# Kernel tuning notes

Measured on AMD Instinct MI355X. Metric: run time of the kernel, lower is better.

The kernel has to match this reference:

```python
import jax, jax.numpy as jnp
import numpy as np

NUM_CLASSES = 21
TOP_K = 200
CONF_THRESH = 0.01
NMS_THRESH = 0.045
VAR0, VAR1 = 0.1, 0.2  # SSD decode variances
B, N = 128, 8732  # batch, num anchors (SSD300)


def setup_inputs() -> dict:
    key = jax.random.key(0)
    k1, k2, k3 = jax.random.split(key, 3)
    loc = jax.random.normal(k1, (B, N, 4), jnp.float32)
    conf = jax.random.normal(k2, (B, N, NUM_CLASSES), jnp.float32)
    # anchors in center-size form (cx, cy, w, h), values in (0,1)
    anchors = jax.random.uniform(k3, (N, 4), jnp.float32)
    return {"loc": loc, "conf": conf, "anchors": anchors}


def decode(loc, anchors):
    # loc [N,4], anchors [N,4] (cx,cy,w,h) -> corner boxes [N,4]
    cxcy = anchors[:, :2] + loc[:, :2] * VAR0 * anchors[:, 2:]
    wh = anchors[:, 2:] * jnp.exp(loc[:, 2:] * VAR1)
    return jnp.concatenate([cxcy - 0.5 * wh, cxcy + 0.5 * wh], axis=-1)


def pairwise_iou(boxes):
    # boxes [K,4] -> IoU [K,K]
    lt = jnp.maximum(boxes[:, None, :2], boxes[None, :, :2])
    rb = jnp.minimum(boxes[:, None, 2:], boxes[None, :, 2:])
    wh = jnp.clip(rb - lt, 0.0)
    inter = wh[..., 0] * wh[..., 1]
    area = (boxes[:, 2] - boxes[:, 0]) * (boxes[:, 3] - boxes[:, 1])
    return inter / (area[:, None] + area[None, :] - inter + 1e-12)


def nms_one_class(scores, boxes):
    # scores [N], boxes [N,4] -> packed [TOP_K, 5] (score, x1,y1,x2,y2)
    masked = jnp.where(scores > CONF_THRESH, scores, 0.0)
    top_s, idx = jax.lax.top_k(masked, TOP_K)
    top_b = boxes[idx]                      # [K,4]
    iou = pairwise_iou(top_b)               # [K,K]
    ar = jnp.arange(TOP_K)
    def body(i, keep):
        sup = keep[i] & (iou[i] > NMS_THRESH) & (ar > i)
        return keep & ~sup
    keep = jax.lax.fori_loop(0, TOP_K, body, top_s > CONF_THRESH)
    # pack kept detections to the front (stable sort preserves score order)
    order = jnp.argsort(jnp.logical_not(keep))
    ent = jnp.concatenate([top_s[:, None], top_b], axis=-1)[order]
    return jnp.where(keep[order][:, None], ent, 0.0)


def reference(loc, conf, anchors):
    probs = jax.nn.softmax(conf, axis=-1)   # [B,N,C]
    def per_image(loc_i, probs_i):
        boxes = decode(loc_i, anchors)      # [N,4]
        return jax.vmap(lambda s: nms_one_class(s, boxes))(probs_i.T)  # [C,K,5]
    out = jax.vmap(per_image)(loc, probs)   # [B,C,K,5]
    return out.at[:, 0].set(0.0)            # class 0 = background, left zero
```

## Files before the change

### kernel.cpp

```cpp
#include <hip/hip_runtime.h>
#include <math.h>

#pragma clang fp contract(off)

#define NB 128
#define NA 8732
#define NC 21
#define TOPK 200
#define BCAP 512
#define CONF_T 0.01
#define NMS_T 0.045
#define NQ (NA / 4)
#define HSIZE 1024

__device__ __forceinline__ double exact_score_cf(const float* __restrict__ conf,
                                                 int b, int i, int c) {
  const float* row = conf + ((size_t)b * NA + i) * NC;
  float r[NC];
#pragma unroll
  for (int k = 0; k < NC; ++k) r[k] = row[k];
  float mx = r[0];
#pragma unroll
  for (int k = 1; k < NC; ++k) mx = fmaxf(mx, r[k]);
  double d = 0.0;
#pragma unroll
  for (int k = 0; k < NC; ++k) d += exp((double)r[k] - (double)mx);
  double s = exp((double)r[c] - (double)mx) / d;
  return (s > CONF_T) ? s : 0.0;
}

__device__ __forceinline__ double exact_score_aux(const float* __restrict__ conf,
                                                  const float* __restrict__ mxa,
                                                  const double* __restrict__ da,
                                                  int b, int i, int c) {
  size_t r = (size_t)b * NA + i;
  double v = (double)conf[r * NC + c];
  double m = (double)mxa[r];
  double s = exp(v - m) / da[r];
  return (s > CONF_T) ? s : 0.0;
}

__device__ __forceinline__ double exact_score(const float* __restrict__ conf,
                                              const float* __restrict__ mxa,
                                              const double* __restrict__ da,
                                              int use_aux, int b, int i, int c) {
  if (use_aux) return exact_score_aux(conf, mxa, da, b, i, c);
  return exact_score_cf(conf, b, i, c);
}

__device__ __forceinline__ void decode64(const float* __restrict__ loc,
                                         const float* __restrict__ anchors,
                                         int b, int ai, double* o) {
  const float* lp = loc + ((size_t)b * NA + ai) * 4;
  const float* ap = anchors + (size_t)ai * 4;
  double l0 = (double)lp[0], l1 = (double)lp[1];
  double l2 = (double)lp[2], l3 = (double)lp[3];
  double a0 = (double)ap[0], a1 = (double)ap[1];
  double a2 = (double)ap[2], a3 = (double)ap[3];
  double cx = a0 + (l0 * 0.1) * a2;
  double cy = a1 + (l1 * 0.1) * a3;
  double w = a2 * exp(l2 * 0.2);
  double h = a3 * exp(l3 * 0.2);
  o[0] = cx - 0.5 * w; o[1] = cy - 0.5 * h;
  o[2] = cx + 0.5 * w; o[3] = cy + 0.5 * h;
}

__device__ __forceinline__ bool entBefore(double sa, int ia, double sb, int ib) {
  return (sa > sb) || (sa == sb && ia < ib);
}

__device__ __forceinline__ int kbucket(unsigned key) {
  if (key == 0u) return -1;
  int x = (int)(key >> 16) - 0x3C00 + 1;
  if (x < 1) x = 1;
  if (x > HSIZE - 1) x = HSIZE - 1;
  return x;
}

__global__ __launch_bounds__(256) void k_prep(const float* __restrict__ conf,
                                              float* __restrict__ scores,
                                              float* __restrict__ mxout,
                                              double* __restrict__ dout,
                                              int do_aux) {
  __shared__ float rows[256 * NC];
  int base = blockIdx.x * 256;
  const float4* src = (const float4*)(conf + (size_t)base * NC);
  float4* dst = (float4*)rows;
  for (int t = threadIdx.x; t < (256 * NC) / 4; t += 256) dst[t] = src[t];
  __syncthreads();
  int g = base + threadIdx.x;
  const float* row = rows + threadIdx.x * NC;
  float v[NC];
#pragma unroll
  for (int k = 0; k < NC; ++k) v[k] = row[k];
  float mx = v[0];
#pragma unroll
  for (int k = 1; k < NC; ++k) mx = fmaxf(mx, v[k]);
  float e[NC], s = 0.0f;
#pragma unroll
  for (int k = 0; k < NC; ++k) {
    e[k] = expf(v[k] - mx);
    s += e[k];
  }
  float inv = 1.0f / s;
  int b = g / NA, i = g - b * NA;
#pragma unroll
  for (int cc = 1; cc < NC; ++cc) {
    float sc = e[cc] * inv;
    scores[(size_t)(b * (NC - 1) + (cc - 1)) * NA + i] = (sc > 0.0099f) ? sc : 0.0f;
  }
  if (do_aux) {
    double d = 0.0;
#pragma unroll
    for (int k = 0; k < NC; ++k) d += exp((double)v[k] - (double)mx);
    mxout[g] = mx;
    dout[g] = d;
  }
}

__global__ __launch_bounds__(256, 8) void k_fast(const float* __restrict__ loc,
                                                 const float* __restrict__ conf,
                                                 const float* __restrict__ anchors,
                                                 const float* __restrict__ scores,
                                                 const float* __restrict__ mxa,
                                                 const double* __restrict__ da,
                                                 float* __restrict__ out,
                                                 int use_aux) {
  int id = blockIdx.x;
  int xcd = id & 7, slot = id >> 3;
  int c = slot % NC;
  int b = (slot / NC) * 8 + xcd;
  int tid = threadIdx.x;
  float* outbase = out + ((size_t)(b * NC + c)) * TOPK * 5;

  if (c == 0) {
    for (int k = tid; k < TOPK * 5; k += 256) outbase[k] = 0.0f;
    return;
  }

  __shared__ unsigned hist[HSIZE];
  __shared__ unsigned chunk[256];
  __shared__ unsigned chunk2[32];
  union U2 {
    struct { double bnds[BCAP]; int bndi[BCAP]; } bb;
    double dbox[TOPK][4];
  };
  __shared__ U2 u2;
  __shared__ float4 fbox[TOPK];
  __shared__ float farea[TOPK];
  __shared__ double ssel[256];
  __shared__ int isel[256];
  __shared__ unsigned keepw[7];
  __shared__ int ctl_cnt, ctl_m, ctl_n1, ctl_kneed, ctl_lo, ctl_hi, ctl_k;
  __shared__ unsigned ctl_pref;

  const float4* sc4 =
      (const float4*)(scores + (size_t)(b * (NC - 1) + (c - 1)) * NA);

  for (int t = tid; t < HSIZE; t += 256) hist[t] = 0u;
  if (tid == 0) { ctl_cnt = 0; ctl_m = 0; }
  __syncthreads();
  for (int q = tid; q < NQ; q += 256) {
    float4 k4 = sc4[q];
    unsigned kb[4] = {__float_as_uint(k4.x), __float_as_uint(k4.y),
                      __float_as_uint(k4.z), __float_as_uint(k4.w)};
#pragma unroll
    for (int t = 0; t < 4; ++t) {
      int idx = kbucket(kb[t]);
      if (idx >= 0) atomicAdd(&hist[idx], 1u);
    }
  }
  __syncthreads();

  {
    unsigned csum = 0;
#pragma unroll
    for (int j = 0; j < 4; ++j) csum += hist[tid * 4 + j];
    chunk[tid] = csum;
  }
  __syncthreads();
  if (tid < 32) {
    unsigned s = 0;
#pragma unroll
    for (int j = 0; j < 8; ++j) s += chunk[tid * 8 + j];
    chunk2[tid] = s;
  }
  __syncthreads();
  if (tid == 0) {
    unsigned cum = 0;
    int t2 = -1;
    for (int t = 31; t >= 0; --t) {
      unsigned h = chunk2[t];
      if (cum + h >= (unsigned)TOPK) { t2 = t; break; }
      cum += h;
    }
    if (t2 < 0) {
      ctl_lo = 1; ctl_hi = 0; ctl_n1 = (int)cum; ctl_kneed = TOPK - (int)cum;
    } else {
      int tc = t2 * 8;
      for (int t = t2 * 8 + 7; t >= t2 * 8; --t) {
        unsigned h = chunk[t];
        if (cum + h >= (unsigned)TOPK) { tc = t; break; }
        cum += h;
      }
      int D = tc * 4;
      for (int j = tc * 4 + 3; j >= tc * 4; --j) {
        unsigned h = hist[j];
        if (cum + h >= (unsigned)TOPK) { D = j; break; }
        cum += h;
      }
      int hi = (D + 1 < HSIZE) ? D + 1 : D;
      int lo = (D - 1 >= 1) ? D - 1 : D;
      unsigned hup = (hi > D) ? hist[hi] : 0u;
      ctl_lo = lo; ctl_hi = hi;
      ctl_n1 = (int)(cum - hup);
      ctl_kneed = TOPK - ctl_n1;
    }
  }
  __syncthreads();
  int lo = ctl_lo, hi = ctl_hi, n1 = ctl_n1, kneed = ctl_kneed;

  {
    unsigned tCert = (unsigned)(0x3C00 + hi) << 16;
    unsigned tBnd = (unsigned)(0x3BFF + lo) << 16;
    for (int q = tid; q < NQ; q += 256) {
      float4 k4 = sc4[q];
      unsigned kb[4] = {__float_as_uint(k4.x), __float_as_uint(k4.y),
                        __float_as_uint(k4.z), __float_as_uint(k4.w)};
#pragma unroll
      for (int t = 0; t < 4; ++t) {
        unsigned key = kb[t];
        if (key >= tCert) {
          int p = atomicAdd(&ctl_cnt, 1);
          if (p < 256) isel[p] = q * 4 + t;
        } else if (key >= tBnd) {
          int p = atomicAdd(&ctl_m, 1);
          if (p < BCAP) u2.bb.bndi[p] = q * 4 + t;
        }
      }
    }
  }
  __syncthreads();
  int m = (hi > 0) ? ctl_m : 0;

  if (hi > 0 && m > BCAP) {
    if (tid == 0) { ctl_k = TOPK; ctl_pref = 0u; }
    __syncthreads();
    for (int shift = 24; shift >= 0; shift -= 8) {
      hist[tid] = 0u;
      __syncthreads();
      unsigned pref = ctl_pref;
      for (int q = tid; q < NQ; q += 256) {
        float4 k4 = sc4[q];
        unsigned kb[4] = {__float_as_uint(k4.x), __float_as_uint(k4.y),
                          __float_as_uint(k4.z), __float_as_uint(k4.w)};
#pragma unroll
        for (int t = 0; t < 4; ++t) {
          unsigned key = kb[t];
          if (key == 0u) continue;
          bool match = (shift == 24) || ((key >> (shift + 8)) == (pref >> (shift + 8)));
          if (match) atomicAdd(&hist[(key >> shift) & 255u], 1u);
        }
      }
      __syncthreads();
      if (tid == 0) {
        int k = ctl_k;
        unsigned cum = 0;
        int d = 255;
        for (; d > 0; --d) {
          unsigned h = hist[d];
          if (cum + h >= (unsigned)k) break;
          cum += h;
        }
        ctl_k = k - (int)cum;
        ctl_pref = pref | ((unsigned)d << shift);
      }
      __syncthreads();
    }
    unsigned Tf = ctl_pref;
    kneed = ctl_k;
    n1 = TOPK - kneed;
    if (tid == 0) { ctl_cnt = 0; ctl_m = 0; }
    __syncthreads();
    for (int q = tid; q < NQ; q += 256) {
      float4 k4 = sc4[q];
      unsigned kb[4] = {__float_as_uint(k4.x), __float_as_uint(k4.y),
                        __float_as_uint(k4.z), __float_as_uint(k4.w)};
#pragma unroll
      for (int t = 0; t < 4; ++t) {
        unsigned key = kb[t];
        if (key > Tf) {
          int p = atomicAdd(&ctl_cnt, 1);
          if (p < 256) isel[p] = q * 4 + t;
        } else if (key == Tf) {
          int p = atomicAdd(&ctl_m, 1);
          if (p < BCAP) u2.bb.bndi[p] = q * 4 + t;
        }
      }
    }
    __syncthreads();
    m = ctl_m;
    if (m > BCAP) m = BCAP;
  }

  if (hi > 0) {
    for (int q = tid; q < m; q += 256)
      u2.bb.bnds[q] = exact_score(conf, mxa, da, use_aux, b, u2.bb.bndi[q], c);
    __syncthreads();
    for (int q = tid; q < m; q += 256) {
      double sq = u2.bb.bnds[q];
      int iq = u2.bb.bndi[q];
      int rank = 0;
      for (int r = 0; r < m; ++r)
        if (entBefore(u2.bb.bnds[r], u2.bb.bndi[r], sq, iq)) ++rank;
      if (rank < kneed) { isel[n1 + rank] = iq; ssel[n1 + rank] = sq; }
    }
  } else {
    for (int j = n1 + tid; j < TOPK; j += 256) {
      isel[j] = j - n1;
      ssel[j] = 0.0;
    }
  }
  __syncthreads();

  if (tid < TOPK) {
    if (tid < n1) ssel[tid] = exact_score(conf, mxa, da, use_aux, b, isel[tid], c);
  } else {
    ssel[tid] = -1.0;
    isel[tid] = 0x7fffffff;
  }

  for (int kk = 2; kk <= 256; kk <<= 1) {
    for (int j = kk >> 1; j > 0; j >>= 1) {
      __syncthreads();
      int ixj = tid ^ j;
      if (ixj > tid) {
        double s1 = ssel[tid], s2 = ssel[ixj];
        int i1 = isel[tid], i2 = isel[ixj];
        bool up = ((tid & kk) == 0);
        bool sw = up ? entBefore(s2, i2, s1, i1) : entBefore(s1, i1, s2, i2);
        if (sw) {
          ssel[tid] = s2; ssel[ixj] = s1;
          isel[tid] = i2; isel[ixj] = i1;
        }
      }
    }
  }
  __syncthreads();

  double dx1 = 0, dy1 = 0, dx2 = 0, dy2 = 0;
  if (tid < TOPK) {
    double bx[4];
    decode64(loc, anchors, b, isel[tid], bx);
    dx1 = bx[0]; dy1 = bx[1]; dx2 = bx[2]; dy2 = bx[3];
    fbox[tid] = make_float4((float)dx1, (float)dy1, (float)dx2, (float)dy2);
    farea[tid] = (float)((dx2 - dx1) * (dy2 - dy1));
    u2.dbox[tid][0] = dx1; u2.dbox[tid][1] = dy1;
    u2.dbox[tid][2] = dx2; u2.dbox[tid][3] = dy2;
  }
  __syncthreads();

  if (tid < 64) {
    int l = tid;
    unsigned kr = 0u;
    float4 ob[4]; float oa[4];
#pragma unroll
    for (int q = 0; q < 4; ++q) {
      int j = l + 64 * q;
      if (j < TOPK) {
        if (ssel[j] > CONF_T) kr |= 1u << q;
        ob[q] = fbox[j];
        oa[q] = farea[j];
      } else {
        ob[q] = make_float4(0.0f, 0.0f, 0.0f, 0.0f);
        oa[q] = 0.0f;
      }
    }
    int cur = 0;
    while (cur < TOPK) {
      unsigned long long ms0 = __ballot((int)(kr & 1u));
      unsigned long long ms1 = __ballot((int)(kr & 2u));
      unsigned long long ms2 = __ballot((int)(kr & 4u));
      unsigned long long ms3 = __ballot((int)(kr & 8u));
      int q0 = cur >> 6;
      int sh = cur & 63;
      unsigned long long below = sh ? ((1ull << sh) - 1ull) : 0ull;
      unsigned long long t0 = (q0 == 0) ? (ms0 & ~below) : 0ull;
      unsigned long long t1 = (q0 < 1) ? ms1 : ((q0 == 1) ? (ms1 & ~below) : 0ull);
      unsigned long long t2 = (q0 < 2) ? ms2 : ((q0 == 2) ? (ms2 & ~below) : 0ull);
      unsigned long long t3 = (q0 < 3) ? ms3 : (ms3 & ~below);
      int i = TOPK;
      if (t0) i = __ffsll(t0) - 1;
      else if (t1) i = 64 + __ffsll(t1) - 1;
      else if (t2) i = 128 + __ffsll(t2) - 1;
      else if (t3) i = 192 + __ffsll(t3) - 1;
      if (i >= TOPK) break;
      float4 fbi = fbox[i];
      float fai = farea[i];
#pragma unroll
      for (int q = 0; q < 4; ++q) {
        int r = l + 64 * q;
        if (r > i && r < TOPK && ((kr >> q) & 1u)) {
          float lx = fmaxf(fbi.x, ob[q].x), ly = fmaxf(fbi.y, ob[q].y);
          float rx = fminf(fbi.z, ob[q].z), ry = fminf(fbi.w, ob[q].w);
          float iw = fmaxf(rx - lx, 0.0f), ih = fmaxf(ry - ly, 0.0f);
          float inter = iw * ih;
          float uni = fai + oa[q] - inter + 1e-12f;
          float diff = inter - 0.045f * uni;
          bool sup;
          if (fabsf(diff) < 3e-4f * uni) {
            double ix1 = u2.dbox[i][0], iy1 = u2.dbox[i][1];
            double ix2 = u2.dbox[i][2], iy2 = u2.dbox[i][3];
            double jx1 = u2.dbox[r][0], jy1 = u2.dbox[r][1];
            double jx2 = u2.dbox[r][2], jy2 = u2.dbox[r][3];
            double dlx = fmax(ix1, jx1), dly = fmax(iy1, jy1);
            double drx = fmin(ix2, jx2), dry = fmin(iy2, jy2);
            double diw = drx - dlx; if (diw < 0.0) diw = 0.0;
            double dih = dry - dly; if (dih < 0.0) dih = 0.0;
            double dint = diw * dih;
            double dai = (ix2 - ix1) * (iy2 - iy1);
            double daj = (jx2 - jx1) * (jy2 - jy1);
            sup = dint > NMS_T * (dai + daj - dint + 1e-12);
          } else {
            sup = diff > 0.0f;
          }
          if (sup) kr &= ~(1u << q);
        }
      }
      cur = i + 1;
    }
#pragma unroll
    for (int q = 0; q < 4; ++q) {
      unsigned long long bal = __ballot((int)((kr >> q) & 1u));
      if (l == 0) {
        keepw[2 * q] = (unsigned)bal;
        if (2 * q + 1 < 7) keepw[2 * q + 1] = (unsigned)(bal >> 32);
      }
    }
  }
  __syncthreads();

  int nk = 0;
#pragma unroll
  for (int w = 0; w < 7; ++w) nk += __popc(keepw[w]);
  if (tid < TOPK) {
    int j = tid;
    bool kept = (keepw[j >> 5] >> (j & 31)) & 1u;
    if (kept) {
      int pos = 0;
      for (int w = 0; w < (j >> 5); ++w) pos += __popc(keepw[w]);
      pos += __popc(keepw[j >> 5] & ((1u << (j & 31)) - 1u));
      float* o = outbase + (size_t)pos * 5;
      o[0] = (float)ssel[j];
      o[1] = (float)dx1;
      o[2] = (float)dy1;
      o[3] = (float)dx2;
      o[4] = (float)dy2;
    }
    if (j >= nk) {
      float* o = outbase + (size_t)j * 5;
      o[0] = 0.0f; o[1] = 0.0f; o[2] = 0.0f; o[3] = 0.0f; o[4] = 0.0f;
    }
  }
}

__global__ __launch_bounds__(256) void k_main_nf(const float* __restrict__ loc,
                                                 const float* __restrict__ conf,
                                                 const float* __restrict__ anchors,
                                                 float* __restrict__ out) {
  int bc = blockIdx.x;
  int b = bc / NC;
  int c = bc % NC;
  int tid = threadIdx.x;
  float* outbase = out + (size_t)bc * TOPK * 5;
  if (c == 0) {
    for (int k = tid; k < TOPK * 5; k += 256) outbase[k] = 0.0f;
    return;
  }
  union U {
    float sf[NA];
    struct { double box[TOPK][4]; double area[TOPK]; } p2;
  };
  __shared__ U u;
  __shared__ double ssel[256];
  __shared__ int isel[256];
  __shared__ unsigned hist[256];
  __shared__ double bnds[256];
  __shared__ int bndi[256];
  __shared__ int keepL[256];
  __shared__ unsigned long long wmask[4];
  __shared__ int ctl_k, ctl_cnt, ctl_m;
  __shared__ unsigned ctl_pref;

  for (int i = tid; i < NA; i += 256)
    u.sf[i] = (float)exact_score_cf(conf, b, i, c);
  if (tid == 0) { ctl_k = TOPK; ctl_pref = 0u; }
  __syncthreads();
  for (int shift = 24; shift >= 0; shift -= 8) {
    hist[tid] = 0u;
    __syncthreads();
    unsigned pref = ctl_pref;
    for (int i = tid; i < NA; i += 256) {
      unsigned key = __float_as_uint(u.sf[i]);
      bool match = (shift == 24) || ((key >> (shift + 8)) == (pref >> (shift + 8)));
      if (match) atomicAdd(&hist[(key >> shift) & 255u], 1u);
    }
    __syncthreads();
    if (tid == 0) {
      int k = ctl_k;
      unsigned cum = 0;
      int d = 255;
      for (; d > 0; --d) {
        unsigned h = hist[d];
        if (cum + h >= (unsigned)k) break;
        cum += h;
      }
      ctl_k = k - (int)cum;
      ctl_pref = pref | ((unsigned)d << shift);
    }
    __syncthreads();
  }
  unsigned Tf = ctl_pref;
  int kneed = ctl_k;
  int n1 = TOPK - kneed;
  if (tid == 0) { ctl_cnt = 0; ctl_m = 0; }
  __syncthreads();
  for (int i = tid; i < NA; i += 256) {
    unsigned key = __float_as_uint(u.sf[i]);
    if (key > Tf) {
      int p = atomicAdd(&ctl_cnt, 1);
      if (p < 256) isel[p] = i;
    } else if (key == Tf && Tf != 0u) {
      int q = atomicAdd(&ctl_m, 1);
      if (q < 256) bndi[q] = i;
    }
  }
  __syncthreads();
  int zf;
  if (Tf == 0u) {
    zf = n1;
    for (int j = n1 + tid; j < TOPK; j += 256) isel[j] = j - n1;
  } else {
    zf = TOPK;
    int m = ctl_m;
    if (m > 256) m = 256;
    if (tid < m) bnds[tid] = exact_score_cf(conf, b, bndi[tid], c);
    __syncthreads();
    if (tid < m) {
      double sq = bnds[tid];
      int iq = bndi[tid];
      int rank = 0;
      for (int r = 0; r < m; ++r)
        if (entBefore(bnds[r], bndi[r], sq, iq)) ++rank;
      if (rank < kneed) isel[n1 + rank] = iq;
    }
  }
  __syncthreads();
  if (tid < TOPK) {
    ssel[tid] = (tid < zf) ? exact_score_cf(conf, b, isel[tid], c) : 0.0;
  } else {
    ssel[tid] = -1.0;
    isel[tid] = 0x7fffffff;
  }
  for (int kk = 2; kk <= 256; kk <<= 1) {
    for (int j = kk >> 1; j > 0; j >>= 1) {
      __syncthreads();
      int ixj = tid ^ j;
      if (ixj > tid) {
        double s1 = ssel[tid], s2 = ssel[ixj];
        int i1 = isel[tid], i2 = isel[ixj];
        bool up = ((tid & kk) == 0);
        bool sw = up ? entBefore(s2, i2, s1, i1) : entBefore(s1, i1, s2, i2);
        if (sw) {
          ssel[tid] = s2; ssel[ixj] = s1;
          isel[tid] = i2; isel[ixj] = i1;
        }
      }
    }
  }
  __syncthreads();
  if (tid < TOPK) {
    double bx[4];
    decode64(loc, anchors, b, isel[tid], bx);
    u.p2.box[tid][0] = bx[0]; u.p2.box[tid][1] = bx[1];
    u.p2.box[tid][2] = bx[2]; u.p2.box[tid][3] = bx[3];
    u.p2.area[tid] = (bx[2] - bx[0]) * (bx[3] - bx[1]);
  }
  __syncthreads();
  double mx1 = 0, my1 = 0, mx2 = 0, my2 = 0, mar = 0;
  if (tid < TOPK) {
    mx1 = u.p2.box[tid][0]; my1 = u.p2.box[tid][1];
    mx2 = u.p2.box[tid][2]; my2 = u.p2.box[tid][3];
    mar = u.p2.area[tid];
  }
  keepL[tid] = (tid < TOPK) && (ssel[tid] > CONF_T);
  __syncthreads();
  for (int i = 0; i < TOPK; ++i) {
    int ki = keepL[i];
    if (ki && tid > i && tid < TOPK && keepL[tid]) {
      double lx = fmax(u.p2.box[i][0], mx1);
      double ly = fmax(u.p2.box[i][1], my1);
      double rx = fmin(u.p2.box[i][2], mx2);
      double ry = fmin(u.p2.box[i][3], my2);
      double iw = rx - lx; if (iw < 0.0) iw = 0.0;
      double ih = ry - ly; if (ih < 0.0) ih = 0.0;
      double inter = iw * ih;
      double iou = inter / (u.p2.area[i] + mar - inter + 1e-12);
      if (iou > NMS_T) keepL[tid] = 0;
    }
    __syncthreads();
  }
  bool kj = (tid < TOPK) && (keepL[tid] != 0);
  unsigned long long bal = __ballot((int)kj);
  int wave = tid >> 6, lane = tid & 63;
  if (lane == 0) wmask[wave] = bal;
  __syncthreads();
  int nk = 0;
#pragma unroll
  for (int w = 0; w < 4; ++w) nk += __popcll(wmask[w]);
  if (kj) {
    int pos = 0;
    for (int w = 0; w < wave; ++w) pos += __popcll(wmask[w]);
    pos += __popcll(bal & ((1ull << lane) - 1ull));
    float* o = outbase + (size_t)pos * 5;
    o[0] = (float)ssel[tid];
    o[1] = (float)u.p2.box[tid][0];
    o[2] = (float)u.p2.box[tid][1];
    o[3] = (float)u.p2.box[tid][2];
    o[4] = (float)u.p2.box[tid][3];
  }
  if (tid < TOPK && tid >= nk) {
    float* o = outbase + (size_t)tid * 5;
    o[0] = 0.0f; o[1] = 0.0f; o[2] = 0.0f; o[3] = 0.0f; o[4] = 0.0f;
  }
}

extern "C" void kernel_launch(void* const* d_in, const int* in_sizes, int n_in,
                              void* d_out, int out_size, void* d_ws, size_t ws_size,
                              hipStream_t stream) {
  const float* loc = (const float*)d_in[0];
  const float* conf = (const float*)d_in[1];
  const float* anchors = (const float*)d_in[2];
  float* out = (float*)d_out;

  const size_t SC_BYTES = (size_t)NB * (NC - 1) * NA * sizeof(float);
  const size_t MX_BYTES = (size_t)NB * NA * sizeof(float);
  const size_t D_BYTES = (size_t)NB * NA * sizeof(double);

  if (ws_size >= SC_BYTES + MX_BYTES + D_BYTES) {
    float* scores = (float*)d_ws;
    float* mxa = (float*)((char*)d_ws + SC_BYTES);
    double* da = (double*)((char*)d_ws + SC_BYTES + MX_BYTES);
    k_prep<<<(NB * NA) / 256, 256, 0, stream>>>(conf, scores, mxa, da, 1);
    k_fast<<<NB * NC, 256, 0, stream>>>(loc, conf, anchors, scores, mxa, da, out, 1);
  } else if (ws_size >= SC_BYTES) {
    float* scores = (float*)d_ws;
    k_prep<<<(NB * NA) / 256, 256, 0, stream>>>(conf, scores, nullptr, nullptr, 0);
    k_fast<<<NB * NC, 256, 0, stream>>>(loc, conf, anchors, scores, nullptr, nullptr, out, 0);
  } else {
    k_main_nf<<<NB * NC, 256, 0, stream>>>(loc, conf, anchors, out);
  }
}
```

Before: 132.2 us.

## Replace bitonic sort of top-k with histogram bucket placement and in-bucket ranking

Computes suffix sums of the score histogram so each certain candidate is scattered straight into its bucket's slot range. A small within-bucket rank then gives its final position, replacing the 36-stage bitonic sort with its many barriers. A verification pass checks ordering and falls back to a serial insertion sort if any inversion is found. The histogram is also shrunk to 904 bins to fit the actual key range. The change adds suffix-sum work, a second histogram clear and extra barriers, and packs bucket ids into the upper bits of isel.

```diff
diff --git a/kernel.cpp b/kernel.cpp
--- a/kernel.cpp
+++ b/kernel.cpp
@@ -11,7 +11,10 @@
 #define CONF_T 0.01
 #define NMS_T 0.045
 #define NQ (NA / 4)
-#define HSIZE 1024
+#define HSIZE 904
+#define CHN 226
+#define CHPAD 232
+#define CH2N 29
 
 __device__ __forceinline__ double exact_score_cf(const float* __restrict__ conf,
                                                  int b, int i, int c) {
@@ -127,9 +130,9 @@
                                                  float* __restrict__ out,
                                                  int use_aux) {
   int id = blockIdx.x;
-  int xcd = id & 7, slot = id >> 3;
-  int c = slot % NC;
-  int b = (slot / NC) * 8 + xcd;
+  int xcd = id & 7, slot0 = id >> 3;
+  int c = slot0 % NC;
+  int b = (slot0 / NC) * 8 + xcd;
   int tid = threadIdx.x;
   float* outbase = out + ((size_t)(b * NC + c)) * TOPK * 5;
 
@@ -139,27 +142,32 @@
   }
 
   __shared__ unsigned hist[HSIZE];
-  __shared__ unsigned chunk[256];
+  __shared__ unsigned chunk[CHPAD];
   __shared__ unsigned chunk2[32];
   union U2 {
     struct { double bnds[BCAP]; int bndi[BCAP]; } bb;
     double dbox[TOPK][4];
   };
   __shared__ U2 u2;
-  __shared__ float4 fbox[TOPK];
-  __shared__ float farea[TOPK];
+  union U3 {
+    unsigned suf[HSIZE];
+    struct { float4 fbox[TOPK]; float farea[TOPK]; } fb;
+  };
+  __shared__ U3 u3;
   __shared__ double ssel[256];
   __shared__ int isel[256];
   __shared__ unsigned keepw[7];
-  __shared__ int ctl_cnt, ctl_m, ctl_n1, ctl_kneed, ctl_lo, ctl_hi, ctl_k;
+  __shared__ int ctl_cnt, ctl_m, ctl_n1, ctl_kneed, ctl_lo, ctl_hi, ctl_k, ctl_fix;
   __shared__ unsigned ctl_pref;
 
   const float4* sc4 =
       (const float4*)(scores + (size_t)(b * (NC - 1) + (c - 1)) * NA);
 
   for (int t = tid; t < HSIZE; t += 256) hist[t] = 0u;
-  if (tid == 0) { ctl_cnt = 0; ctl_m = 0; }
-  __syncthreads();
+  for (int t = tid; t < TOPK; t += 256) isel[t] = 0;
+  if (tid == 0) { ctl_cnt = 0; ctl_m = 0; ctl_fix = 0; }
+  __syncthreads();
+
   for (int q = tid; q < NQ; q += 256) {
     float4 k4 = sc4[q];
     unsigned kb[4] = {__float_as_uint(k4.x), __float_as_uint(k4.y),
@@ -172,24 +180,28 @@
   }
   __syncthreads();
 
-  {
+  if (tid < CHN) {
     unsigned csum = 0;
 #pragma unroll
     for (int j = 0; j < 4; ++j) csum += hist[tid * 4 + j];
     chunk[tid] = csum;
-  }
-  __syncthreads();
-  if (tid < 32) {
+  } else if (tid < CHPAD) {
+    chunk[tid] = 0u;
+  }
+  __syncthreads();
+
+  if (tid < CH2N) {
     unsigned s = 0;
 #pragma unroll
     for (int j = 0; j < 8; ++j) s += chunk[tid * 8 + j];
     chunk2[tid] = s;
   }
   __syncthreads();
+
   if (tid == 0) {
     unsigned cum = 0;
     int t2 = -1;
-    for (int t = 31; t >= 0; --t) {
+    for (int t = CH2N - 1; t >= 0; --t) {
       unsigned h = chunk2[t];
       if (cum + h >= (unsigned)TOPK) { t2 = t; break; }
       cum += h;
@@ -216,9 +228,31 @@
       ctl_n1 = (int)(cum - hup);
       ctl_kneed = TOPK - ctl_n1;
     }
+    unsigned run = 0;
+    for (int w = CH2N - 1; w >= 0; --w) {
+      unsigned h = chunk2[w];
+      chunk2[w] = run;
+      run += h;
+    }
   }
   __syncthreads();
   int lo = ctl_lo, hi = ctl_hi, n1 = ctl_n1, kneed = ctl_kneed;
+
+  if (tid < CHN) {
+    unsigned s = chunk2[tid >> 3];
+    int ge = ((tid >> 3) + 1) << 3;
+    for (int u = tid + 1; u < ge; ++u) s += chunk[u];
+    int b0 = tid * 4;
+    unsigned h3 = hist[b0 + 3], h2 = hist[b0 + 2], h1 = hist[b0 + 1];
+    u3.suf[b0 + 3] = s;
+    u3.suf[b0 + 2] = s + h3;
+    u3.suf[b0 + 1] = s + h3 + h2;
+    u3.suf[b0 + 0] = s + h3 + h2 + h1;
+  }
+  __syncthreads();
+
+  for (int t = tid; t < HSIZE; t += 256) hist[t] = 0u;
+  __syncthreads();
 
   {
     unsigned tCert = (unsigned)(0x3C00 + hi) << 16;
@@ -231,8 +265,9 @@
       for (int t = 0; t < 4; ++t) {
         unsigned key = kb[t];
         if (key >= tCert) {
-          int p = atomicAdd(&ctl_cnt, 1);
-          if (p < 256) isel[p] = q * 4 + t;
+          int bk = kbucket(key);
+          int slot = (int)u3.suf[bk] + (int)atomicAdd(&hist[bk], 1u);
+          if (slot < TOPK) isel[slot] = (bk << 16) | (q * 4 + t);
         } else if (key >= tBnd) {
           int p = atomicAdd(&ctl_m, 1);
           if (p < BCAP) u2.bb.bndi[p] = q * 4 + t;
@@ -301,9 +336,6 @@
     __syncthreads();
     m = ctl_m;
     if (m > BCAP) m = BCAP;
-  }
-
-  if (hi > 0) {
     for (int q = tid; q < m; q += 256)
       u2.bb.bnds[q] = exact_score(conf, mxa, da, use_aux, b, u2.bb.bndi[q], c);
     __syncthreads();
@@ -315,46 +347,105 @@
         if (entBefore(u2.bb.bnds[r], u2.bb.bndi[r], sq, iq)) ++rank;
       if (rank < kneed) { isel[n1 + rank] = iq; ssel[n1 + rank] = sq; }
     }
+    __syncthreads();
+    if (tid < TOPK) {
+      if (tid < n1) ssel[tid] = exact_score(conf, mxa, da, use_aux, b, isel[tid], c);
+    } else {
+      ssel[tid] = -1.0;
+      isel[tid] = 0x7fffffff;
+    }
+    for (int kk = 2; kk <= 256; kk <<= 1) {
+      for (int j = kk >> 1; j > 0; j >>= 1) {
+        __syncthreads();
+        int ixj = tid ^ j;
+        if (ixj > tid) {
+          double s1 = ssel[tid], s2 = ssel[ixj];
+          int i1 = isel[tid], i2 = isel[ixj];
+          bool up = ((tid & kk) == 0);
+          bool sw = up ? entBefore(s2, i2, s1, i1) : entBefore(s1, i1, s2, i2);
+          if (sw) {
+            ssel[tid] = s2; ssel[ixj] = s1;
+            isel[tid] = i2; isel[ixj] = i1;
+          }
+        }
+      }
+    }
+    __syncthreads();
   } else {
-    for (int j = n1 + tid; j < TOPK; j += 256) {
-      isel[j] = j - n1;
-      ssel[j] = 0.0;
-    }
-  }
-  __syncthreads();
-
-  if (tid < TOPK) {
-    if (tid < n1) ssel[tid] = exact_score(conf, mxa, da, use_aux, b, isel[tid], c);
-  } else {
-    ssel[tid] = -1.0;
-    isel[tid] = 0x7fffffff;
-  }
-
-  for (int kk = 2; kk <= 256; kk <<= 1) {
-    for (int j = kk >> 1; j > 0; j >>= 1) {
+    if (tid < n1)
+      ssel[tid] = exact_score(conf, mxa, da, use_aux, b, isel[tid] & 0xFFFF, c);
+    if (hi > 0) {
+      for (int q = tid; q < m; q += 256)
+        u2.bb.bnds[q] = exact_score(conf, mxa, da, use_aux, b, u2.bb.bndi[q], c);
+    }
+    __syncthreads();
+    double myS = 0.0;
+    int myI = 0, myPos = -1;
+    if (tid < n1) {
+      int packed = isel[tid];
+      int bk = packed >> 16;
+      myI = packed & 0xFFFF;
+      myS = ssel[tid];
+      int base = (int)u3.suf[bk];
+      int len = (int)u3.suf[bk - 1] - base;
+      int r = 0;
+      for (int u = base; u < base + len; ++u) {
+        if (u == tid) continue;
+        double ps = ssel[u];
+        int pI = isel[u] & 0xFFFF;
+        if (entBefore(ps, pI, myS, myI)) ++r;
+      }
+      myPos = base + r;
+    }
+    if (hi > 0) {
+      for (int q = tid; q < m; q += 256) {
+        double sq = u2.bb.bnds[q];
+        int iq = u2.bb.bndi[q];
+        int rank = 0;
+        for (int r = 0; r < m; ++r)
+          if (entBefore(u2.bb.bnds[r], u2.bb.bndi[r], sq, iq)) ++rank;
+        if (rank < kneed) { isel[n1 + rank] = iq; ssel[n1 + rank] = sq; }
+      }
+    } else {
+      for (int j = n1 + tid; j < TOPK; j += 256) {
+        isel[j] = j - n1;
+        ssel[j] = 0.0;
+      }
+    }
+    __syncthreads();
+    if (myPos >= 0 && myPos < TOPK) { ssel[myPos] = myS; isel[myPos] = myI; }
+    __syncthreads();
+    if (tid < 64) {
+      bool inv = false;
+      for (int j = tid + 1; j < TOPK; j += 64)
+        if (entBefore(ssel[j], isel[j], ssel[j - 1], isel[j - 1])) inv = true;
+      unsigned long long bal = __ballot((int)inv);
+      if (tid == 0 && bal != 0ull) ctl_fix = 1;
+    }
+    __syncthreads();
+    if (ctl_fix) {
+      if (tid == 0) {
+        for (int a = 1; a < TOPK; ++a) {
+          double s = ssel[a];
+          int ii = isel[a];
+          int p = a - 1;
+          while (p >= 0 && entBefore(s, ii, ssel[p], isel[p])) {
+            ssel[p + 1] = ssel[p]; isel[p + 1] = isel[p]; --p;
+          }
+          ssel[p + 1] = s; isel[p + 1] = ii;
+        }
+      }
       __syncthreads();
-      int ixj = tid ^ j;
-      if (ixj > tid) {
-        double s1 = ssel[tid], s2 = ssel[ixj];
-        int i1 = isel[tid], i2 = isel[ixj];
-        bool up = ((tid & kk) == 0);
-        bool sw = up ? entBefore(s2, i2, s1, i1) : entBefore(s1, i1, s2, i2);
-        if (sw) {
-          ssel[tid] = s2; ssel[ixj] = s1;
-          isel[tid] = i2; isel[ixj] = i1;
-        }
-      }
-    }
-  }
-  __syncthreads();
+    }
+  }
 
   double dx1 = 0, dy1 = 0, dx2 = 0, dy2 = 0;
   if (tid < TOPK) {
     double bx[4];
     decode64(loc, anchors, b, isel[tid], bx);
     dx1 = bx[0]; dy1 = bx[1]; dx2 = bx[2]; dy2 = bx[3];
-    fbox[tid] = make_float4((float)dx1, (float)dy1, (float)dx2, (float)dy2);
-    farea[tid] = (float)((dx2 - dx1) * (dy2 - dy1));
+    u3.fb.fbox[tid] = make_float4((float)dx1, (float)dy1, (float)dx2, (float)dy2);
+    u3.fb.farea[tid] = (float)((dx2 - dx1) * (dy2 - dy1));
     u2.dbox[tid][0] = dx1; u2.dbox[tid][1] = dy1;
     u2.dbox[tid][2] = dx2; u2.dbox[tid][3] = dy2;
   }
@@ -369,8 +460,8 @@
       int j = l + 64 * q;
       if (j < TOPK) {
         if (ssel[j] > CONF_T) kr |= 1u << q;
-        ob[q] = fbox[j];
-        oa[q] = farea[j];
+        ob[q] = u3.fb.fbox[j];
+        oa[q] = u3.fb.farea[j];
       } else {
         ob[q] = make_float4(0.0f, 0.0f, 0.0f, 0.0f);
         oa[q] = 0.0f;
@@ -395,8 +486,8 @@
       else if (t2) i = 128 + __ffsll(t2) - 1;
       else if (t3) i = 192 + __ffsll(t3) - 1;
       if (i >= TOPK) break;
-      float4 fbi = fbox[i];
-      float fai = farea[i];
+      float4 fbi = u3.fb.fbox[i];
+      float fai = u3.fb.farea[i];
 #pragma unroll
       for (int q = 0; q < 4; ++q) {
         int r = l + 64 * q;
```

After: 119.8 us. 1.1x faster.
